# Performance work log

Hardware: AMD Instinct MI355X
Metric: run time of the kernel (lower is better)

## Reference

```python
import jax, jax.numpy as jnp
import numpy as np

B, F, C, H, W, D = 4, 2, 16, 48, 160, 96
EPS = 1e-7


def setup_inputs() -> dict:
    key = jax.random.key(0)
    k0, k1, k2 = jax.random.split(key, 3)
    current_feats = jax.random.normal(k0, (B, C, H, W), jnp.float32)
    lookup_feats = jax.random.normal(k1, (B, F, C, H, W), jnp.float32)
    # near-identity relative poses so warps land mostly in-frame
    relative_poses = jnp.eye(4, dtype=jnp.float32)[None, None] \
        + 0.02 * jax.random.normal(k2, (B, F, 4, 4), jnp.float32)
    fx, fy, cx, cy = 0.58 * W, 1.92 * H, 0.5 * W, 0.5 * H
    Kmat = jnp.array([[fx, 0., cx, 0.], [0., fy, cy, 0.],
                      [0., 0., 1., 0.], [0., 0., 0., 1.]], jnp.float32)
    K = jnp.broadcast_to(Kmat, (B, 4, 4))
    invK = jnp.broadcast_to(jnp.linalg.inv(Kmat), (B, 4, 4))
    depth_bins = jnp.linspace(2.0, 20.0, D).astype(jnp.float32)
    return {"current_feats": current_feats, "lookup_feats": lookup_feats,
            "relative_poses": relative_poses, "K": K, "invK": invK,
            "depth_bins": depth_bins}


def _pix_coords():
    # homogeneous pixel grid [3, H*W], matching BackprojectDepth
    xs, ys = jnp.meshgrid(jnp.arange(W, dtype=jnp.float32),
                          jnp.arange(H, dtype=jnp.float32), indexing='xy')
    return jnp.stack([xs.ravel(), ys.ravel(), jnp.ones(H * W, jnp.float32)], 0)


def _interior_mask():
    m = jnp.zeros((H, W), jnp.float32).at[2:-2, 2:-2].set(1.0)
    return m.reshape(H * W)


def _bilinear_zeros(img, x, y):
    """grid_sample(mode=bilinear, padding=zeros, align_corners=True).
    img [C,H,W]; x,y [D,HW] in pixel coords. Returns [D,HW] ... [C,D,HW]."""
    x0 = jnp.floor(x); y0 = jnp.floor(y)
    fx = (x - x0)[None]; fy = (y - y0)[None]  # [1,D,HW]
    x0i = x0.astype(jnp.int32); y0i = y0.astype(jnp.int32)
    flat = img.reshape(C, H * W)

    def tap(xi, yi):
        valid = ((xi >= 0) & (xi < W) & (yi >= 0) & (yi < H)).astype(img.dtype)
        idx = jnp.clip(yi, 0, H - 1) * W + jnp.clip(xi, 0, W - 1)
        return flat[:, idx] * valid[None]  # [C,D,HW]

    return (tap(x0i, y0i) * (1 - fx) * (1 - fy)
            + tap(x0i + 1, y0i) * fx * (1 - fy)
            + tap(x0i, y0i + 1) * (1 - fx) * fy
            + tap(x0i + 1, y0i + 1) * fx * fy)


def _per_pair(cur, lf, T, Kb, invKb, depth_bins):
    # cur [C,H,W], lf [C,H,W], T/Kb/invKb [4,4]
    pix = _pix_coords()                              # [3,HW]
    rays = invKb[:3, :3] @ pix                       # [3,HW]
    pts = depth_bins[:, None, None] * rays[None]     # [D,3,HW]
    pts4 = jnp.concatenate([pts, jnp.ones((D, 1, H * W), pts.dtype)], 1)
    P = (Kb @ T)[:3]                                 # [3,4]
    cam = jnp.einsum('ij,djn->din', P, pts4)         # [D,3,HW]
    z = cam[:, 2] + EPS
    px = cam[:, 0] / z                               # [D,HW] pixel x
    py = cam[:, 1] / z                               # [D,HW] pixel y
    # torch normalizes to [-1,1] then grid_sample(align_corners=True)
    # un-normalizes back to exactly px,py; sample directly.
    warped = _bilinear_zeros(lf, px, py)             # [C,D,HW]
    edge = ((px >= 2.0) & (px <= W - 2) & (py >= 2.0) & (py <= H - 2))
    mask = edge.astype(cur.dtype) * _interior_mask()[None]  # [D,HW]
    diffs = jnp.abs(warped - cur.reshape(C, 1, H * W)).mean(0) * mask
    return diffs.reshape(D, H, W)


def reference(current_feats, lookup_feats, relative_poses, K, invK, depth_bins):
    pair = jax.vmap(_per_pair, in_axes=(None, 0, 0, None, None, None))  # over frames
    diffs = jax.vmap(pair, in_axes=(0, 0, 0, 0, 0, None))(
        current_feats, lookup_feats, relative_poses, K, invK, depth_bins)  # [B,F,D,H,W]
    valid = (relative_poses.sum((-1, -2)) != 0).astype(diffs.dtype)  # skip zero poses
    diffs = diffs * valid[:, :, None, None, None]
    cost = diffs.sum(1)                                   # [B,D,H,W]
    counts = (diffs > 0).astype(diffs.dtype).sum(1)
    cost = cost / (counts + 1e-7)
    missing = (cost == 0).astype(cost.dtype)
    cost = cost * (1 - missing) + cost.max(1, keepdims=True) * missing
    return cost, missing
```

## Files before the change

kernel.cpp:

```cpp
#include <hip/hip_runtime.h>
#include <hip/hip_fp16.h>

#define B_ 4
#define F_ 2
#define C_ 16
#define H_ 48
#define W_ 160
#define D_ 96
#define HW_ (H_*W_)
#define PIX_ 64
#define GRP_ 16
#define BINS_ (D_/GRP_)
#define NCHUNK_ (HW_/PIX_)

__global__ __launch_bounds__(256) void prep_kernel(
    const float* __restrict__ cur, const float* __restrict__ look,
    const float* __restrict__ poses, const float* __restrict__ Kmat,
    __half* __restrict__ curH, __half* __restrict__ lookH,
    float* __restrict__ mats)
{
  int tid = threadIdx.x;
  int bid = blockIdx.x;
  if (bid == 0 && tid < B_*F_) {
    int t = tid, b = t / F_;
    const float* T  = poses + t*16;
    const float* Kb = Kmat + b*16;
    float sum = 0.f;
    #pragma unroll
    for (int i = 0; i < 16; ++i) sum += T[i];
    #pragma unroll
    for (int i = 0; i < 3; ++i) {
      #pragma unroll
      for (int j = 0; j < 4; ++j) {
        float v = 0.f;
        #pragma unroll
        for (int k = 0; k < 4; ++k) v += Kb[i*4+k] * T[k*4+j];
        mats[t*16 + i*4 + j] = v;
      }
    }
    mats[t*16 + 12] = (sum != 0.f) ? 1.f : 0.f;
  }
  int px_l = tid & 127;
  int h    = tid >> 7;
  int gp   = bid*128 + px_l;
  const float* src;
  __half* dst;
  int hw, c0 = h*8;
  if (gp < B_*HW_) {
    hw = gp % HW_;
    int s = gp / HW_;
    src = cur + (size_t)s*C_*HW_ + hw;
    dst = curH + (size_t)gp*C_ + c0;
  } else {
    int j = gp - B_*HW_;
    hw = j % HW_;
    int s = j / HW_;
    src = look + (size_t)s*C_*HW_ + hw;
    dst = lookH + (size_t)j*C_ + c0;
  }
  __half2 hh[4];
  #pragma unroll
  for (int j = 0; j < 4; ++j)
    hh[j] = __floats2half2_rn(src[(size_t)(c0+2*j)*HW_], src[(size_t)(c0+2*j+1)*HW_]);
  *reinterpret_cast<uint4*>(dst) = *reinterpret_cast<uint4*>(&hh[0]);
}

__global__ __launch_bounds__(1024, 4) void fused_kernel(
    const __half* __restrict__ curH, const __half* __restrict__ lookH,
    const float* __restrict__ mats, const float* __restrict__ invK,
    const float* __restrict__ dbins,
    float* __restrict__ cost, float* __restrict__ missing)
{
  int tid = threadIdx.x;
  int pix = tid & (PIX_-1);
  int grp = tid >> 6;
  int bid = blockIdx.x;
  int chunk = bid % NCHUNK_;
  int b = bid / NCHUNK_;
  int hw = chunk*PIX_ + pix;
  int x = hw % W_, y = hw / W_;
  size_t obase = ((size_t)(b*D_ + grp*BINS_))*HW_ + hw;

  float res[BINS_];
  #pragma unroll
  for (int dd = 0; dd < BINS_; ++dd) res[dd] = 0.f;
  float lmax = 0.f;
  bool interior = (x >= 2 && x < W_-2 && y >= 2 && y < H_-2);
  if (interior) {
    const float* iK = invK + b*16;
    float xf = (float)x, yf = (float)y;
    float r0 = iK[0]*xf + iK[1]*yf + iK[2];
    float r1 = iK[4]*xf + iK[5]*yf + iK[6];
    float r2 = iK[8]*xf + iK[9]*yf + iK[10];
    __half2 cc2[8];
    {
      const uint4* cur4 = reinterpret_cast<const uint4*>(curH + (size_t)(b*HW_ + hw)*C_);
      *reinterpret_cast<uint4*>(&cc2[0]) = cur4[0];
      *reinterpret_cast<uint4*>(&cc2[4]) = cur4[1];
    }
    float diffs0[BINS_];
    #pragma unroll
    for (int f = 0; f < F_; ++f) {
      const float* Mt = mats + (b*F_+f)*16;
      float M0=Mt[0], M1=Mt[1], M2 =Mt[2],  M3 =Mt[3];
      float M4=Mt[4], M5=Mt[5], M6 =Mt[6],  M7 =Mt[7];
      float M8=Mt[8], M9=Mt[9], M10=Mt[10], M11=Mt[11];
      float valid = Mt[12];
      const __half* fbase = lookH + (size_t)((b*F_+f)*HW_)*C_;
      #pragma unroll
      for (int dd = 0; dd < BINS_; ++dd) {
        float dep = dbins[grp*BINS_ + dd];
        float p0 = dep*r0, p1 = dep*r1, p2 = dep*r2;
        float camx = M0*p0 + M1*p1 + M2 *p2 + M3;
        float camy = M4*p0 + M5*p1 + M6 *p2 + M7;
        float camz = M8*p0 + M9*p1 + M10*p2 + M11;
        float z  = camz + 1e-7f;
        float px = camx / z;
        float py = camy / z;
        bool ok = (valid != 0.f) && (px >= 2.f) && (px <= (float)(W_-2))
                                 && (py >= 2.f) && (py <= (float)(H_-2));
        float x0 = floorf(px), y0 = floorf(py);
        float fx = px - x0, fy = py - y0;
        fx = fminf(fmaxf(fx, 0.f), 1.f);
        fy = fminf(fmaxf(fy, 0.f), 1.f);
        int xi = min(max((int)x0, 0), W_-2);
        int yi = min(max((int)y0, 0), H_-2);
        const __half* base = fbase + ((size_t)(yi*W_ + xi))*C_;
        uint4 t[8];
        {
          const uint4* rr0 = reinterpret_cast<const uint4*>(base);
          const uint4* rr1 = reinterpret_cast<const uint4*>(base + W_*C_);
          #pragma unroll
          for (int i = 0; i < 4; ++i) t[i]   = rr0[i];
          #pragma unroll
          for (int i = 0; i < 4; ++i) t[4+i] = rr1[i];
        }
        __half2 w00h = __float2half2_rn((1.f-fx)*(1.f-fy));
        __half2 w10h = __float2half2_rn(fx*(1.f-fy));
        __half2 w01h = __float2half2_rn((1.f-fx)*fy);
        __half2 w11h = __float2half2_rn(fx*fy);
        const __half2* a00 = reinterpret_cast<const __half2*>(&t[0]);
        const __half2* a10 = reinterpret_cast<const __half2*>(&t[2]);
        const __half2* a01 = reinterpret_cast<const __half2*>(&t[4]);
        const __half2* a11 = reinterpret_cast<const __half2*>(&t[6]);
        __half2 acc0 = __float2half2_rn(0.f);
        __half2 acc1 = __float2half2_rn(0.f);
        #pragma unroll
        for (int i = 0; i < 8; ++i) {
          __half2 v = __hmul2(w00h, a00[i]);
          v = __hfma2(w10h, a10[i], v);
          v = __hfma2(w01h, a01[i], v);
          v = __hfma2(w11h, a11[i], v);
          __half2 dsub = __habs2(__hsub2(v, cc2[i]));
          if (i & 1) acc1 = __hadd2(acc1, dsub);
          else       acc0 = __hadd2(acc0, dsub);
        }
        float2 f0 = __half22float2(acc0);
        float2 f1 = __half22float2(acc1);
        float s = (f0.x + f0.y) + (f1.x + f1.y);
        float diffs = s * (1.f/16.f);
        diffs = ok ? diffs : 0.f;
        if (f == 0) {
          diffs0[dd] = diffs;
        } else {
          float c0v = diffs0[dd];
          float cnt = ((c0v > 0.f) ? 1.f : 0.f) + ((diffs > 0.f) ? 1.f : 0.f);
          float r = (c0v + diffs) / (cnt + 1e-7f);
          res[dd] = r;
          lmax = fmaxf(lmax, r);
        }
      }
    }
  }

  __shared__ float lmaxs[GRP_][PIX_];
  lmaxs[grp][pix] = lmax;
  __syncthreads();
  float pmax = lmaxs[0][pix];
  #pragma unroll
  for (int g = 1; g < GRP_; ++g) pmax = fmaxf(pmax, lmaxs[g][pix]);

  #pragma unroll
  for (int dd = 0; dd < BINS_; ++dd) {
    size_t o = obase + (size_t)dd*HW_;
    float v = res[dd];
    float miss = (v == 0.f) ? 1.f : 0.f;
    cost[o]    = miss ? pmax : v;
    missing[o] = miss;
  }
}

extern "C" void kernel_launch(void* const* d_in, const int* in_sizes, int n_in,
                              void* d_out, int out_size, void* d_ws, size_t ws_size,
                              hipStream_t stream) {
  const float* cur   = (const float*)d_in[0];
  const float* look  = (const float*)d_in[1];
  const float* poses = (const float*)d_in[2];
  const float* Km    = (const float*)d_in[3];
  const float* invK  = (const float*)d_in[4];
  const float* dbins = (const float*)d_in[5];

  float* out_cost = (float*)d_out;
  float* out_miss = out_cost + (size_t)B_*D_*HW_;

  char*   ws    = (char*)d_ws;
  float*  mats  = (float*)ws;
  __half* curH  = (__half*)(ws + 1024);
  __half* lookH = (__half*)(ws + 1024 + (size_t)B_*HW_*C_*2);

  prep_kernel<<<(B_*HW_ + B_*F_*HW_)/128, 256, 0, stream>>>(
      cur, look, poses, Km, curH, lookH, mats);
  fused_kernel<<<B_*NCHUNK_, 1024, 0, stream>>>(
      curH, lookH, mats, invK, dbins, out_cost, out_miss);
}
```

Measured before the change: 44.76 us.

## Stage warped source rows in LDS per block and halve depth groups

Each block first computes the range of source rows its pixels' projections touch for each frame. When that range fits in 12 rows, it copies those rows of the fp16 lookup features into shared memory, and the bilinear gathers then read from LDS instead of global memory. Otherwise it falls back to global loads. The block size also drops to 512 threads, with 8 depth groups of 12 bins each. The change adds a projection pre-pass, atomics and barriers, plus about 61 KB of shared memory, which may limit occupancy.

Result: slower. 65.26 us (+45.8%).

```diff
diff --git a/kernel.cpp b/kernel.cpp
--- a/kernel.cpp
+++ b/kernel.cpp
@@ -9,9 +9,11 @@
 #define D_ 96
 #define HW_ (H_*W_)
 #define PIX_ 64
-#define GRP_ 16
+#define GRP_ 8
 #define BINS_ (D_/GRP_)
 #define NCHUNK_ (HW_/PIX_)
+#define NROWS_ 12
+#define ROWU4_ (W_*2)
 
 __global__ __launch_bounds__(256) void prep_kernel(
     const float* __restrict__ cur, const float* __restrict__ look,
@@ -65,12 +67,16 @@
   *reinterpret_cast<uint4*>(dst) = *reinterpret_cast<uint4*>(&hh[0]);
 }
 
-__global__ __launch_bounds__(1024, 4) void fused_kernel(
+__global__ __launch_bounds__(512, 4) void fused_kernel(
     const __half* __restrict__ curH, const __half* __restrict__ lookH,
     const float* __restrict__ mats, const float* __restrict__ invK,
     const float* __restrict__ dbins,
     float* __restrict__ cost, float* __restrict__ missing)
 {
+  __shared__ uint4 stage[NROWS_*ROWU4_];
+  __shared__ float lmaxs[GRP_][PIX_];
+  __shared__ int s_ymin, s_ymax;
+
   int tid = threadIdx.x;
   int pix = tid & (PIX_-1);
   int grp = tid >> 6;
@@ -80,37 +86,72 @@
   int hw = chunk*PIX_ + pix;
   int x = hw % W_, y = hw / W_;
   size_t obase = ((size_t)(b*D_ + grp*BINS_))*HW_ + hw;
+  bool interior = (x >= 2 && x < W_-2 && y >= 2 && y < H_-2);
+
+  const float* iK = invK + b*16;
+  float xf = (float)x, yf = (float)y;
+  float r0 = iK[0]*xf + iK[1]*yf + iK[2];
+  float r1 = iK[4]*xf + iK[5]*yf + iK[6];
+  float r2 = iK[8]*xf + iK[9]*yf + iK[10];
+  __half2 cc2[8];
+  {
+    const uint4* cur4 = reinterpret_cast<const uint4*>(curH + (size_t)(b*HW_ + hw)*C_);
+    *reinterpret_cast<uint4*>(&cc2[0]) = cur4[0];
+    *reinterpret_cast<uint4*>(&cc2[4]) = cur4[1];
+  }
+  float dep[BINS_];
+  #pragma unroll
+  for (int dd = 0; dd < BINS_; ++dd) dep[dd] = dbins[grp*BINS_ + dd];
 
   float res[BINS_];
   #pragma unroll
   for (int dd = 0; dd < BINS_; ++dd) res[dd] = 0.f;
+  float diffs0[BINS_];
+  #pragma unroll
+  for (int dd = 0; dd < BINS_; ++dd) diffs0[dd] = 0.f;
   float lmax = 0.f;
-  bool interior = (x >= 2 && x < W_-2 && y >= 2 && y < H_-2);
-  if (interior) {
-    const float* iK = invK + b*16;
-    float xf = (float)x, yf = (float)y;
-    float r0 = iK[0]*xf + iK[1]*yf + iK[2];
-    float r1 = iK[4]*xf + iK[5]*yf + iK[6];
-    float r2 = iK[8]*xf + iK[9]*yf + iK[10];
-    __half2 cc2[8];
-    {
-      const uint4* cur4 = reinterpret_cast<const uint4*>(curH + (size_t)(b*HW_ + hw)*C_);
-      *reinterpret_cast<uint4*>(&cc2[0]) = cur4[0];
-      *reinterpret_cast<uint4*>(&cc2[4]) = cur4[1];
-    }
-    float diffs0[BINS_];
-    #pragma unroll
-    for (int f = 0; f < F_; ++f) {
-      const float* Mt = mats + (b*F_+f)*16;
-      float M0=Mt[0], M1=Mt[1], M2 =Mt[2],  M3 =Mt[3];
-      float M4=Mt[4], M5=Mt[5], M6 =Mt[6],  M7 =Mt[7];
-      float M8=Mt[8], M9=Mt[9], M10=Mt[10], M11=Mt[11];
-      float valid = Mt[12];
-      const __half* fbase = lookH + (size_t)((b*F_+f)*HW_)*C_;
+
+  for (int f = 0; f < F_; ++f) {
+    const float* Mt = mats + (b*F_+f)*16;
+    float M0=Mt[0], M1=Mt[1], M2 =Mt[2],  M3 =Mt[3];
+    float M4=Mt[4], M5=Mt[5], M6 =Mt[6],  M7 =Mt[7];
+    float M8=Mt[8], M9=Mt[9], M10=Mt[10], M11=Mt[11];
+    float valid = Mt[12];
+    const __half* fbase = lookH + (size_t)((b*F_+f)*HW_)*C_;
+
+    int my_ymin = H_, my_ymax = -1;
+    if (interior) {
       #pragma unroll
       for (int dd = 0; dd < BINS_; ++dd) {
-        float dep = dbins[grp*BINS_ + dd];
-        float p0 = dep*r0, p1 = dep*r1, p2 = dep*r2;
+        float p0 = dep[dd]*r0, p1 = dep[dd]*r1, p2 = dep[dd]*r2;
+        float camy = M4*p0 + M5*p1 + M6 *p2 + M7;
+        float camz = M8*p0 + M9*p1 + M10*p2 + M11;
+        float z  = camz + 1e-7f;
+        float py = camy / z;
+        float y0 = floorf(py);
+        int yi = min(max((int)y0, 0), H_-2);
+        my_ymin = min(my_ymin, yi);
+        my_ymax = max(my_ymax, yi);
+      }
+    }
+    if (tid == 0) { s_ymin = H_; s_ymax = -1; }
+    __syncthreads();
+    atomicMin(&s_ymin, my_ymin);
+    atomicMax(&s_ymax, my_ymax);
+    __syncthreads();
+    int ymin = s_ymin, ymax = s_ymax;
+    int nr = ymax + 2 - ymin;
+    bool lds_use = (ymax >= 0) && (nr <= NROWS_);
+    if (lds_use) {
+      const uint4* fsrc = reinterpret_cast<const uint4*>(fbase) + (size_t)ymin*ROWU4_;
+      for (int i = tid; i < nr*ROWU4_; i += 512) stage[i] = fsrc[i];
+    }
+    __syncthreads();
+
+    if (interior) {
+      #pragma unroll
+      for (int dd = 0; dd < BINS_; ++dd) {
+        float p0 = dep[dd]*r0, p1 = dep[dd]*r1, p2 = dep[dd]*r2;
         float camx = M0*p0 + M1*p1 + M2 *p2 + M3;
         float camy = M4*p0 + M5*p1 + M6 *p2 + M7;
         float camz = M8*p0 + M9*p1 + M10*p2 + M11;
@@ -125,11 +166,16 @@
         fy = fminf(fmaxf(fy, 0.f), 1.f);
         int xi = min(max((int)x0, 0), W_-2);
         int yi = min(max((int)y0, 0), H_-2);
-        const __half* base = fbase + ((size_t)(yi*W_ + xi))*C_;
         uint4 t[8];
-        {
-          const uint4* rr0 = reinterpret_cast<const uint4*>(base);
-          const uint4* rr1 = reinterpret_cast<const uint4*>(base + W_*C_);
+        if (lds_use) {
+          int bi = ((yi - ymin)*W_ + xi)*2;
+          #pragma unroll
+          for (int i = 0; i < 4; ++i) t[i]   = stage[bi + i];
+          #pragma unroll
+          for (int i = 0; i < 4; ++i) t[4+i] = stage[bi + ROWU4_ + i];
+        } else {
+          const uint4* rr0 = reinterpret_cast<const uint4*>(fbase + ((size_t)(yi*W_ + xi))*C_);
+          const uint4* rr1 = rr0 + (W_*C_)/8;
           #pragma unroll
           for (int i = 0; i < 4; ++i) t[i]   = rr0[i];
           #pragma unroll
@@ -171,9 +217,9 @@
         }
       }
     }
-  }
-
-  __shared__ float lmaxs[GRP_][PIX_];
+    __syncthreads();
+  }
+
   lmaxs[grp][pix] = lmax;
   __syncthreads();
   float pmax = lmaxs[0][pix];
@@ -210,6 +256,6 @@
 
   prep_kernel<<<(B_*HW_ + B_*F_*HW_)/128, 256, 0, stream>>>(
       cur, look, poses, Km, curH, lookH, mats);
-  fused_kernel<<<B_*NCHUNK_, 1024, 0, stream>>>(
+  fused_kernel<<<B_*NCHUNK_, 512, 0, stream>>>(
       curH, lookH, mats, invK, dbins, out_cost, out_miss);
 }
```

## Split lookup features into two 8-channel planes and halve threads per block

Applied to the files above, without the earlier changes.

The lookup feature buffer is repacked into two planes of 8 half-channels per pixel. Horizontally adjacent bilinear taps now sit in consecutive 16-byte words within each plane, so each gather is a pair of adjacent 16-byte loads per row per plane. Depth groups drop from 16 to 8, giving 512 threads per block with 12 bins each, and depth values are preloaded into registers. More bins per thread raises register pressure and lowers parallelism per pixel chunk.

Result: slower. 52.75 us (+17.9%).

```diff
diff --git a/kernel.cpp b/kernel.cpp
--- a/kernel.cpp
+++ b/kernel.cpp
@@ -9,14 +9,14 @@
 #define D_ 96
 #define HW_ (H_*W_)
 #define PIX_ 64
-#define GRP_ 16
+#define GRP_ 8
 #define BINS_ (D_/GRP_)
 #define NCHUNK_ (HW_/PIX_)
 
 __global__ __launch_bounds__(256) void prep_kernel(
     const float* __restrict__ cur, const float* __restrict__ look,
     const float* __restrict__ poses, const float* __restrict__ Kmat,
-    __half* __restrict__ curH, __half* __restrict__ lookH,
+    __half* __restrict__ curH, __half* __restrict__ lookP,
     float* __restrict__ mats)
 {
   int tid = threadIdx.x;
@@ -56,7 +56,7 @@
     hw = j % HW_;
     int s = j / HW_;
     src = look + (size_t)s*C_*HW_ + hw;
-    dst = lookH + (size_t)j*C_ + c0;
+    dst = lookP + ((size_t)(s*2 + h)*HW_ + hw)*8;
   }
   __half2 hh[4];
   #pragma unroll
@@ -65,8 +65,8 @@
   *reinterpret_cast<uint4*>(dst) = *reinterpret_cast<uint4*>(&hh[0]);
 }
 
-__global__ __launch_bounds__(1024, 4) void fused_kernel(
-    const __half* __restrict__ curH, const __half* __restrict__ lookH,
+__global__ __launch_bounds__(512, 4) void fused_kernel(
+    const __half* __restrict__ curH, const __half* __restrict__ lookP,
     const float* __restrict__ mats, const float* __restrict__ invK,
     const float* __restrict__ dbins,
     float* __restrict__ cost, float* __restrict__ missing)
@@ -98,6 +98,10 @@
       *reinterpret_cast<uint4*>(&cc2[0]) = cur4[0];
       *reinterpret_cast<uint4*>(&cc2[4]) = cur4[1];
     }
+    float dep[BINS_];
+    #pragma unroll
+    for (int dd = 0; dd < BINS_; ++dd) dep[dd] = dbins[grp*BINS_ + dd];
+
     float diffs0[BINS_];
     #pragma unroll
     for (int f = 0; f < F_; ++f) {
@@ -106,11 +110,11 @@
       float M4=Mt[4], M5=Mt[5], M6 =Mt[6],  M7 =Mt[7];
       float M8=Mt[8], M9=Mt[9], M10=Mt[10], M11=Mt[11];
       float valid = Mt[12];
-      const __half* fbase = lookH + (size_t)((b*F_+f)*HW_)*C_;
+      const __half* pl0 = lookP + (size_t)((b*F_+f)*2)*HW_*8;
+      const __half* pl1 = pl0 + (size_t)HW_*8;
       #pragma unroll
       for (int dd = 0; dd < BINS_; ++dd) {
-        float dep = dbins[grp*BINS_ + dd];
-        float p0 = dep*r0, p1 = dep*r1, p2 = dep*r2;
+        float p0 = dep[dd]*r0, p1 = dep[dd]*r1, p2 = dep[dd]*r2;
         float camx = M0*p0 + M1*p1 + M2 *p2 + M3;
         float camy = M4*p0 + M5*p1 + M6 *p2 + M7;
         float camz = M8*p0 + M9*p1 + M10*p2 + M11;
@@ -125,33 +129,47 @@
         fy = fminf(fmaxf(fy, 0.f), 1.f);
         int xi = min(max((int)x0, 0), W_-2);
         int yi = min(max((int)y0, 0), H_-2);
-        const __half* base = fbase + ((size_t)(yi*W_ + xi))*C_;
+        int offu4 = yi*W_ + xi;
         uint4 t[8];
         {
-          const uint4* rr0 = reinterpret_cast<const uint4*>(base);
-          const uint4* rr1 = reinterpret_cast<const uint4*>(base + W_*C_);
-          #pragma unroll
-          for (int i = 0; i < 4; ++i) t[i]   = rr0[i];
-          #pragma unroll
-          for (int i = 0; i < 4; ++i) t[4+i] = rr1[i];
+          const uint4* q0 = reinterpret_cast<const uint4*>(pl0) + offu4;
+          const uint4* q1 = reinterpret_cast<const uint4*>(pl1) + offu4;
+          t[0] = q0[0];      t[1] = q0[1];
+          t[2] = q0[W_];     t[3] = q0[W_+1];
+          t[4] = q1[0];      t[5] = q1[1];
+          t[6] = q1[W_];     t[7] = q1[W_+1];
         }
         __half2 w00h = __float2half2_rn((1.f-fx)*(1.f-fy));
         __half2 w10h = __float2half2_rn(fx*(1.f-fy));
         __half2 w01h = __float2half2_rn((1.f-fx)*fy);
         __half2 w11h = __float2half2_rn(fx*fy);
-        const __half2* a00 = reinterpret_cast<const __half2*>(&t[0]);
-        const __half2* a10 = reinterpret_cast<const __half2*>(&t[2]);
-        const __half2* a01 = reinterpret_cast<const __half2*>(&t[4]);
-        const __half2* a11 = reinterpret_cast<const __half2*>(&t[6]);
+        const __half2* b00 = reinterpret_cast<const __half2*>(&t[0]);
+        const __half2* b10 = reinterpret_cast<const __half2*>(&t[1]);
+        const __half2* b01 = reinterpret_cast<const __half2*>(&t[2]);
+        const __half2* b11 = reinterpret_cast<const __half2*>(&t[3]);
+        const __half2* c00 = reinterpret_cast<const __half2*>(&t[4]);
+        const __half2* c10 = reinterpret_cast<const __half2*>(&t[5]);
+        const __half2* c01 = reinterpret_cast<const __half2*>(&t[6]);
+        const __half2* c11 = reinterpret_cast<const __half2*>(&t[7]);
         __half2 acc0 = __float2half2_rn(0.f);
         __half2 acc1 = __float2half2_rn(0.f);
         #pragma unroll
-        for (int i = 0; i < 8; ++i) {
-          __half2 v = __hmul2(w00h, a00[i]);
-          v = __hfma2(w10h, a10[i], v);
-          v = __hfma2(w01h, a01[i], v);
-          v = __hfma2(w11h, a11[i], v);
+        for (int i = 0; i < 4; ++i) {
+          __half2 v = __hmul2(w00h, b00[i]);
+          v = __hfma2(w10h, b10[i], v);
+          v = __hfma2(w01h, b01[i], v);
+          v = __hfma2(w11h, b11[i], v);
           __half2 dsub = __habs2(__hsub2(v, cc2[i]));
+          if (i & 1) acc1 = __hadd2(acc1, dsub);
+          else       acc0 = __hadd2(acc0, dsub);
+        }
+        #pragma unroll
+        for (int i = 0; i < 4; ++i) {
+          __half2 v = __hmul2(w00h, c00[i]);
+          v = __hfma2(w10h, c10[i], v);
+          v = __hfma2(w01h, c01[i], v);
+          v = __hfma2(w11h, c11[i], v);
+          __half2 dsub = __habs2(__hsub2(v, cc2[4+i]));
           if (i & 1) acc1 = __hadd2(acc1, dsub);
           else       acc0 = __hadd2(acc0, dsub);
         }
@@ -206,10 +224,10 @@
   char*   ws    = (char*)d_ws;
   float*  mats  = (float*)ws;
   __half* curH  = (__half*)(ws + 1024);
-  __half* lookH = (__half*)(ws + 1024 + (size_t)B_*HW_*C_*2);
+  __half* lookP = (__half*)(ws + 1024 + (size_t)B_*HW_*C_*2);
 
   prep_kernel<<<(B_*HW_ + B_*F_*HW_)/128, 256, 0, stream>>>(
-      cur, look, poses, Km, curH, lookH, mats);
-  fused_kernel<<<B_*NCHUNK_, 1024, 0, stream>>>(
-      curH, lookH, mats, invK, dbins, out_cost, out_miss);
+      cur, look, poses, Km, curH, lookP, mats);
+  fused_kernel<<<B_*NCHUNK_, 512, 0, stream>>>(
+      curH, lookP, mats, invK, dbins, out_cost, out_miss);
 }
```
